# Kernel tuning notes

Measured on AMD Instinct MI355X. Metric: run time of the kernel, lower is better.

Reference implementation:

```python
import jax, jax.numpy as jnp
import numpy as np

ALPHA = 0.2          # LeakyReLU negative slope
NEG_INF = -9e15      # mask value used by the original module


def setup_inputs() -> dict:
    key = jax.random.key(0)
    k1, k2, k3, k4 = jax.random.split(key, 4)
    N, F_IN, F_OUT = 8192, 512, 256
    inp = jax.random.normal(k1, (N, F_IN), dtype=jnp.float32)
    W = jax.random.normal(k2, (F_IN, F_OUT), dtype=jnp.float32) * (1.414 / np.sqrt(F_IN))
    a = jax.random.normal(k3, (2 * F_OUT, 1), dtype=jnp.float32) * (1.414 / np.sqrt(F_OUT))
    adj = jax.random.randint(k4, (N, N), 0, 2, dtype=jnp.int32)
    return {"input": inp, "W": W, "a": a, "adj": adj}


def reference(input, W, a, adj):
    # h: [N, F_out]
    h = input @ W
    F_out = h.shape[1]
    # Original builds a_input[i,j] = concat(h_i, h_j) then matmuls with a.
    # Equivalent: e_ij = leakyrelu(h_i . a[:F] + h_j . a[F:]) without the O(N^2 * 2F) tensor.
    a1 = a[:F_out, 0]   # [F_out]
    a2 = a[F_out:, 0]   # [F_out]
    s1 = h @ a1         # [N]
    s2 = h @ a2         # [N]
    e = jax.nn.leaky_relu(s1[:, None] + s2[None, :], negative_slope=ALPHA)  # [N, N]
    attention = jax.nn.softmax(jnp.where(adj > 0, e, NEG_INF), axis=1)       # [N, N]
    return attention @ h  # [N, F_out]
```

## Files before the change

kernel.cpp:

```cpp
#include <hip/hip_runtime.h>


typedef __attribute__((ext_vector_type(8))) short bf16x8;
typedef __attribute__((ext_vector_type(4))) float fx4;
typedef __attribute__((ext_vector_type(4))) int ix4;
typedef __attribute__((ext_vector_type(2))) unsigned int ux2;

#define NN 8192
#define FIN 512
#define FOUT 256
#define PS 136
#define AROWS 32

__device__ __forceinline__ unsigned short f2bf(float f) {
    unsigned int x = __float_as_uint(f);
    x += 0x7fffu + ((x >> 16) & 1u);
    return (unsigned short)(x >> 16);
}
__device__ __forceinline__ bf16x8 pack8(fx4 a, fx4 b) {
    bf16x8 r;
    r[0] = (short)f2bf(a[0]); r[1] = (short)f2bf(a[1]);
    r[2] = (short)f2bf(a[2]); r[3] = (short)f2bf(a[3]);
    r[4] = (short)f2bf(b[0]); r[5] = (short)f2bf(b[1]);
    r[6] = (short)f2bf(b[2]); r[7] = (short)f2bf(b[3]);
    return r;
}

__global__ void wt_kernel(const float* __restrict__ W,
                          unsigned short* __restrict__ WTt) {
    const int c = threadIdx.x;
    const int k = blockIdx.x;
    WTt[((size_t)(k >> 5) * 256 + c) * 32 + (k & 31)] = f2bf(W[k * FOUT + c]);
}

__global__ __launch_bounds__(256) void prep_kernel(
    const float* __restrict__ X,
    const unsigned short* __restrict__ WTt,
    const float* __restrict__ A,
    unsigned short* __restrict__ hTt,
    float* __restrict__ s1, float* __restrict__ s2)
{
    __shared__ float s1sh[4][16], s2sh[4][16];
    const int tid = threadIdx.x;

    const int w = tid >> 6, l = tid & 63, q = l >> 4, lr = l & 15;
    const int r0 = blockIdx.x * 16;
    const int cbase = w * 64;
    fx4 acc[4] = {};

    for (int kb = 0; kb < FIN; kb += 32) {
        const float* xp = X + (size_t)(r0 + lr) * FIN + kb + q * 8;
        bf16x8 a0 = pack8(*(const fx4*)xp, *(const fx4*)(xp + 4));
#pragma unroll
        for (int tc = 0; tc < 4; ++tc) {
            bf16x8 b = *(const bf16x8*)(WTt + ((size_t)(kb >> 5) * 256 + cbase + tc * 16 + lr) * 32 + q * 8);
            acc[tc] = __builtin_amdgcn_mfma_f32_16x16x32_bf16(a0, b, acc[tc], 0, 0, 0);
        }
    }

    const int jb = r0 >> 5, jo = (r0 & 31) + q * 4;
#pragma unroll
    for (int tc = 0; tc < 4; ++tc) {
        const int c = cbase + tc * 16 + lr;
        ux2 hp;
        hp.x = (unsigned)f2bf(acc[tc][0]) | ((unsigned)f2bf(acc[tc][1]) << 16);
        hp.y = (unsigned)f2bf(acc[tc][2]) | ((unsigned)f2bf(acc[tc][3]) << 16);
        *(ux2*)(hTt + ((size_t)jb * 256 + c) * 32 + jo) = hp;
    }

    float p1[4] = {}, p2[4] = {};
#pragma unroll
    for (int tc = 0; tc < 4; ++tc) {
        const int c = cbase + tc * 16 + lr;
        const float a1v = A[c], a2v = A[FOUT + c];
#pragma unroll
        for (int r = 0; r < 4; ++r) {
            p1[r] += acc[tc][r] * a1v;
            p2[r] += acc[tc][r] * a2v;
        }
    }
#pragma unroll
    for (int r = 0; r < 4; ++r) {
#pragma unroll
        for (int off = 1; off < 16; off <<= 1) {
            p1[r] += __shfl_xor(p1[r], off);
            p2[r] += __shfl_xor(p2[r], off);
        }
        if (lr == 0) { s1sh[w][q * 4 + r] = p1[r]; s2sh[w][q * 4 + r] = p2[r]; }
    }
    __syncthreads();
    if (tid < 16) {
        s1[r0 + tid] = s1sh[0][tid] + s1sh[1][tid] + s1sh[2][tid] + s1sh[3][tid];
        s2[r0 + tid] = s2sh[0][tid] + s2sh[1][tid] + s2sh[2][tid] + s2sh[3][tid];
    }
}

__global__ __launch_bounds__(512) void attn_kernel(
    const int* __restrict__ adj,
    const unsigned short* __restrict__ hTt,
    const float* __restrict__ s1,
    const float* __restrict__ s2,
    float* __restrict__ out)
{
    __shared__ unsigned short P[2][AROWS * PS];
    __shared__ float dsh[AROWS];

    const int tid = threadIdx.x;
    const int r0 = blockIdx.x * AROWS;

    const int prow = tid >> 4;
    const int pq = tid & 15;
    const float s1v = s1[r0 + prow];
    const int* arow = adj + (size_t)(r0 + prow) * NN + pq * 8;
    float denp = 0.f;

    const int w = tid >> 6, l = tid & 63, q = l >> 4, lr = l & 15;
    const int cbase = w * 32;
    fx4 acc[2][2] = {};

    struct LSet { ix4 v0, v1; fx4 s2a, s2b; };
    LSet LA, LB;
    bf16x8 B0[4][2], B1[4][2];

    auto loadP = [&](int kt, LSet& L) {
        const int* ap = arow + kt * 128;
        L.v0 = __builtin_nontemporal_load((const ix4*)ap);
        L.v1 = __builtin_nontemporal_load((const ix4*)(ap + 4));
        L.s2a = *(const fx4*)(s2 + kt * 128 + pq * 8);
        L.s2b = *(const fx4*)(s2 + kt * 128 + pq * 8 + 4);
    };
    auto calcP = [&](int b, const LSet& L) {
        bf16x8 pv;
#pragma unroll
        for (int j = 0; j < 8; ++j) {
            const int aj = (j < 4) ? L.v0[j] : L.v1[j - 4];
            const float s2j = (j < 4) ? L.s2a[j] : L.s2b[j - 4];
            float t = s1v + s2j;
            float e = fmaxf(t, 0.2f * t);
            e = fminf(e, 30.f);
            const float p = (aj != 0) ? __expf(e) : 0.f;
            denp += p;
            pv[j] = (short)f2bf(p);
        }
        *(bf16x8*)(&P[b][prow * PS + pq * 8]) = pv;
    };
    auto loadB = [&](int it, bf16x8 (&B)[4][2]) {
#pragma unroll
        for (int ks = 0; ks < 4; ++ks)
#pragma unroll
            for (int tc = 0; tc < 2; ++tc)
                B[ks][tc] = *(const bf16x8*)(hTt + ((size_t)(it * 4 + ks) * 256 + cbase + tc * 16 + lr) * 32 + q * 8);
    };

    auto ldsBarrier = [&]() {
        asm volatile("s_waitcnt lgkmcnt(0)" ::: "memory");
        __builtin_amdgcn_s_barrier();
    };

    const int ITERS = NN / 128;
    loadP(0, LA);
    calcP(0, LA);
    loadP(1, LA);
    loadB(0, B0);
    ldsBarrier();

    auto body = [&](int it, bf16x8 (&Bc)[4][2], bf16x8 (&Bn)[4][2],
                    LSet& Lc, LSet& Ln) {
        if (it + 1 < ITERS) loadB(it + 1, Bn);
        if (it + 2 < ITERS) loadP(it + 2, Ln);
        const unsigned short* Pb = P[it & 1];
        bf16x8 af0[4], af1[4];
#pragma unroll
        for (int ks = 0; ks < 4; ++ks) {
            af0[ks] = *(const bf16x8*)(Pb + lr * PS + ks * 32 + q * 8);
            af1[ks] = *(const bf16x8*)(Pb + (16 + lr) * PS + ks * 32 + q * 8);
        }
        __builtin_amdgcn_s_setprio(1);
#pragma unroll
        for (int ks = 0; ks < 4; ++ks)
#pragma unroll
            for (int tc = 0; tc < 2; ++tc) {
                acc[0][tc] = __builtin_amdgcn_mfma_f32_16x16x32_bf16(af0[ks], Bc[ks][tc], acc[0][tc], 0, 0, 0);
                acc[1][tc] = __builtin_amdgcn_mfma_f32_16x16x32_bf16(af1[ks], Bc[ks][tc], acc[1][tc], 0, 0, 0);
            }
        __builtin_amdgcn_s_setprio(0);
        if (it + 1 < ITERS) calcP((it + 1) & 1, Lc);
        ldsBarrier();
    };

    for (int it = 0; it < ITERS; it += 2) {
        body(it, B0, B1, LA, LB);
        body(it + 1, B1, B0, LB, LA);
    }

    float v = denp;
    v += __shfl_xor(v, 1);
    v += __shfl_xor(v, 2);
    v += __shfl_xor(v, 4);
    v += __shfl_xor(v, 8);
    if (pq == 0) dsh[prow] = v;
    __syncthreads();

#pragma unroll
    for (int mg = 0; mg < 2; ++mg) {
#pragma unroll
        for (int r = 0; r < 4; ++r) {
            const int row = mg * 16 + q * 4 + r;
            const float dinv = 1.0f / fmaxf(dsh[row], 1e-30f);
#pragma unroll
            for (int tc = 0; tc < 2; ++tc) {
                out[(size_t)(r0 + row) * FOUT + cbase + tc * 16 + lr] = acc[mg][tc][r] * dinv;
            }
        }
    }
}

extern "C" void kernel_launch(void* const* d_in, const int* in_sizes, int n_in,
                              void* d_out, int out_size, void* d_ws, size_t ws_size,
                              hipStream_t stream) {
    const float *X = nullptr, *W = nullptr, *A = nullptr;
    const int* adj = nullptr;
    for (int i = 0; i < n_in; ++i) {
        switch (in_sizes[i]) {
            case NN * FIN:   X = (const float*)d_in[i]; break;
            case FIN * FOUT: W = (const float*)d_in[i]; break;
            case 2 * FOUT:   A = (const float*)d_in[i]; break;
            case NN * NN:    adj = (const int*)d_in[i]; break;
        }
    }
    if (!X) X = (const float*)d_in[0];
    if (!W) W = (const float*)d_in[1];
    if (!A) A = (const float*)d_in[2];
    if (!adj) adj = (const int*)d_in[3];
    float* out = (float*)d_out;

    char* ws = (char*)d_ws;
    float* s1 = (float*)ws;
    float* s2 = (float*)(ws + 32768);
    unsigned short* WTt = (unsigned short*)(ws + 98304);
    unsigned short* hTt = (unsigned short*)(ws + 360448);

    wt_kernel<<<512, 256, 0, stream>>>(W, WTt);
    prep_kernel<<<512, 256, 0, stream>>>(X, WTt, A, hTt, s1, s2);
    attn_kernel<<<NN / AROWS, 512, 0, stream>>>(adj, hTt, s1, s2, out);
}
```

Baseline: 442.4 us.

## Shrink attention tile to 16 rows with 256 threads and single-buffered B

Halves the attention block to 16 rows and 256 threads, so each wave covers 64 output columns (4 MFMA tiles) for one 16-row A fragment instead of two row groups over 32 columns. The B fragments of hTt are no longer double-buffered in registers but loaded at the start of each iteration, and the P computation for the next tile is moved ahead of the MFMAs to overlap it with those loads. This doubles the grid to 512 blocks and cuts register pressure, raising occupancy. The cost is that hTt is re-read twice as many times in total and B load latency is exposed within each iteration.

```diff
diff --git a/kernel.cpp b/kernel.cpp
--- a/kernel.cpp
+++ b/kernel.cpp
@@ -10,7 +10,7 @@
 #define FIN 512
 #define FOUT 256
 #define PS 136
-#define AROWS 32
+#define AROWS 16
 
 __device__ __forceinline__ unsigned short f2bf(float f) {
     unsigned int x = __float_as_uint(f);
@@ -95,7 +95,7 @@
     }
 }
 
-__global__ __launch_bounds__(512) void attn_kernel(
+__global__ __launch_bounds__(256) void attn_kernel(
     const int* __restrict__ adj,
     const unsigned short* __restrict__ hTt,
     const float* __restrict__ s1,
@@ -115,12 +115,12 @@
     float denp = 0.f;
 
     const int w = tid >> 6, l = tid & 63, q = l >> 4, lr = l & 15;
-    const int cbase = w * 32;
-    fx4 acc[2][2] = {};
+    const int cbase = w * 64;
+    fx4 acc[4] = {};
 
     struct LSet { ix4 v0, v1; fx4 s2a, s2b; };
     LSet LA, LB;
-    bf16x8 B0[4][2], B1[4][2];
+    bf16x8 B[4][4];
 
     auto loadP = [&](int kt, LSet& L) {
         const int* ap = arow + kt * 128;
@@ -144,11 +144,11 @@
         }
         *(bf16x8*)(&P[b][prow * PS + pq * 8]) = pv;
     };
-    auto loadB = [&](int it, bf16x8 (&B)[4][2]) {
+    auto loadB = [&](int it) {
 #pragma unroll
         for (int ks = 0; ks < 4; ++ks)
 #pragma unroll
-            for (int tc = 0; tc < 2; ++tc)
+            for (int tc = 0; tc < 4; ++tc)
                 B[ks][tc] = *(const bf16x8*)(hTt + ((size_t)(it * 4 + ks) * 256 + cbase + tc * 16 + lr) * 32 + q * 8);
     };
 
@@ -161,36 +161,30 @@
     loadP(0, LA);
     calcP(0, LA);
     loadP(1, LA);
-    loadB(0, B0);
     ldsBarrier();
 
-    auto body = [&](int it, bf16x8 (&Bc)[4][2], bf16x8 (&Bn)[4][2],
-                    LSet& Lc, LSet& Ln) {
-        if (it + 1 < ITERS) loadB(it + 1, Bn);
+    auto body = [&](int it, LSet& Lc, LSet& Ln) {
+        loadB(it);
         if (it + 2 < ITERS) loadP(it + 2, Ln);
         const unsigned short* Pb = P[it & 1];
-        bf16x8 af0[4], af1[4];
-#pragma unroll
-        for (int ks = 0; ks < 4; ++ks) {
+        bf16x8 af0[4];
+#pragma unroll
+        for (int ks = 0; ks < 4; ++ks)
             af0[ks] = *(const bf16x8*)(Pb + lr * PS + ks * 32 + q * 8);
-            af1[ks] = *(const bf16x8*)(Pb + (16 + lr) * PS + ks * 32 + q * 8);
-        }
+        if (it + 1 < ITERS) calcP((it + 1) & 1, Lc);
         __builtin_amdgcn_s_setprio(1);
 #pragma unroll
         for (int ks = 0; ks < 4; ++ks)
 #pragma unroll
-            for (int tc = 0; tc < 2; ++tc) {
-                acc[0][tc] = __builtin_amdgcn_mfma_f32_16x16x32_bf16(af0[ks], Bc[ks][tc], acc[0][tc], 0, 0, 0);
-                acc[1][tc] = __builtin_amdgcn_mfma_f32_16x16x32_bf16(af1[ks], Bc[ks][tc], acc[1][tc], 0, 0, 0);
-            }
+            for (int tc = 0; tc < 4; ++tc)
+                acc[tc] = __builtin_amdgcn_mfma_f32_16x16x32_bf16(af0[ks], B[ks][tc], acc[tc], 0, 0, 0);
         __builtin_amdgcn_s_setprio(0);
-        if (it + 1 < ITERS) calcP((it + 1) & 1, Lc);
         ldsBarrier();
     };
 
     for (int it = 0; it < ITERS; it += 2) {
-        body(it, B0, B1, LA, LB);
-        body(it + 1, B1, B0, LB, LA);
+        body(it, LA, LB);
+        body(it + 1, LB, LA);
     }
 
     float v = denp;
@@ -202,15 +196,12 @@
     __syncthreads();
 
 #pragma unroll
-    for (int mg = 0; mg < 2; ++mg) {
-#pragma unroll
-        for (int r = 0; r < 4; ++r) {
-            const int row = mg * 16 + q * 4 + r;
-            const float dinv = 1.0f / fmaxf(dsh[row], 1e-30f);
-#pragma unroll
-            for (int tc = 0; tc < 2; ++tc) {
-                out[(size_t)(r0 + row) * FOUT + cbase + tc * 16 + lr] = acc[mg][tc][r] * dinv;
-            }
+    for (int r = 0; r < 4; ++r) {
+        const int row = q * 4 + r;
+        const float dinv = 1.0f / fmaxf(dsh[row], 1e-30f);
+#pragma unroll
+        for (int tc = 0; tc < 4; ++tc) {
+            out[(size_t)(r0 + row) * FOUT + cbase + tc * 16 + lr] = acc[tc][r] * dinv;
         }
     }
 }
@@ -242,5 +233,5 @@
 
     wt_kernel<<<512, 256, 0, stream>>>(W, WTt);
     prep_kernel<<<512, 256, 0, stream>>>(X, WTt, A, hTt, s1, s2);
-    attn_kernel<<<NN / AROWS, 512, 0, stream>>>(adj, hTt, s1, s2, out);
-}
+    attn_kernel<<<NN / AROWS, 256, 0, stream>>>(adj, hTt, s1, s2, out);
+}
```

Result: slower. 478.2 us (+8.1%).

## Prefetch adjacency block into LDS bitmask before attention main loop

Applied to the files above, without the earlier changes.

Before the main loop, each block streams its 32 adjacency rows with wide nontemporal loads and packs them into a 32-bit-per-word bitmask held in LDS (about 33 KB). The softmax-numerator step then reads mask bits from LDS instead of issuing global int loads inside the pipelined loop. This separates the bandwidth-heavy adjacency read from the MFMA loop, but it serialises that read ahead of compute and raises LDS use per block, which may cut occupancy.

```diff
diff --git a/kernel.cpp b/kernel.cpp
--- a/kernel.cpp
+++ b/kernel.cpp
@@ -11,6 +11,7 @@
 #define FOUT 256
 #define PS 136
 #define AROWS 32
+#define MPAD 260
 
 __device__ __forceinline__ unsigned short f2bf(float f) {
     unsigned int x = __float_as_uint(f);
@@ -103,42 +104,60 @@
     float* __restrict__ out)
 {
     __shared__ unsigned short P[2][AROWS * PS];
+    __shared__ unsigned int mlds[AROWS * MPAD];
     __shared__ float dsh[AROWS];
 
     const int tid = threadIdx.x;
     const int r0 = blockIdx.x * AROWS;
+
+#pragma unroll 2
+    for (int s = 0; s < 16; ++s) {
+        const int g = s * 512 + tid;
+        const int row = g >> 8, dw = g & 255;
+        const int* base = adj + (size_t)(r0 + row) * NN + dw * 32;
+        ix4 v[8];
+#pragma unroll
+        for (int k = 0; k < 8; ++k)
+            v[k] = __builtin_nontemporal_load((const ix4*)(base + k * 4));
+        unsigned int m = 0;
+#pragma unroll
+        for (int k = 0; k < 8; ++k)
+#pragma unroll
+            for (int j = 0; j < 4; ++j)
+                m |= (v[k][j] != 0 ? 1u : 0u) << (k * 4 + j);
+        mlds[row * MPAD + dw] = m;
+    }
+    __syncthreads();
 
     const int prow = tid >> 4;
     const int pq = tid & 15;
     const float s1v = s1[r0 + prow];
-    const int* arow = adj + (size_t)(r0 + prow) * NN + pq * 8;
+    const int mshift = (pq & 3) * 8;
     float denp = 0.f;
 
     const int w = tid >> 6, l = tid & 63, q = l >> 4, lr = l & 15;
     const int cbase = w * 32;
     fx4 acc[2][2] = {};
 
-    struct LSet { ix4 v0, v1; fx4 s2a, s2b; };
+    struct LSet { fx4 s2a, s2b; };
     LSet LA, LB;
     bf16x8 B0[4][2], B1[4][2];
 
-    auto loadP = [&](int kt, LSet& L) {
-        const int* ap = arow + kt * 128;
-        L.v0 = __builtin_nontemporal_load((const ix4*)ap);
-        L.v1 = __builtin_nontemporal_load((const ix4*)(ap + 4));
+    auto loadS = [&](int kt, LSet& L) {
         L.s2a = *(const fx4*)(s2 + kt * 128 + pq * 8);
         L.s2b = *(const fx4*)(s2 + kt * 128 + pq * 8 + 4);
     };
-    auto calcP = [&](int b, const LSet& L) {
+    auto calcP = [&](int b, int kt, const LSet& L) {
+        const unsigned int mval = mlds[prow * MPAD + kt * 4 + (pq >> 2)];
+        const unsigned int mbyte = (mval >> mshift) & 0xFFu;
         bf16x8 pv;
 #pragma unroll
         for (int j = 0; j < 8; ++j) {
-            const int aj = (j < 4) ? L.v0[j] : L.v1[j - 4];
             const float s2j = (j < 4) ? L.s2a[j] : L.s2b[j - 4];
             float t = s1v + s2j;
             float e = fmaxf(t, 0.2f * t);
             e = fminf(e, 30.f);
-            const float p = (aj != 0) ? __expf(e) : 0.f;
+            const float p = ((mbyte >> j) & 1u) ? __expf(e) : 0.f;
             denp += p;
             pv[j] = (short)f2bf(p);
         }
@@ -158,16 +177,16 @@
     };
 
     const int ITERS = NN / 128;
-    loadP(0, LA);
-    calcP(0, LA);
-    loadP(1, LA);
+    loadS(0, LA);
+    calcP(0, 0, LA);
+    loadS(1, LA);
     loadB(0, B0);
     ldsBarrier();
 
     auto body = [&](int it, bf16x8 (&Bc)[4][2], bf16x8 (&Bn)[4][2],
                     LSet& Lc, LSet& Ln) {
         if (it + 1 < ITERS) loadB(it + 1, Bn);
-        if (it + 2 < ITERS) loadP(it + 2, Ln);
+        if (it + 2 < ITERS) loadS(it + 2, Ln);
         const unsigned short* Pb = P[it & 1];
         bf16x8 af0[4], af1[4];
 #pragma unroll
@@ -184,7 +203,7 @@
                 acc[1][tc] = __builtin_amdgcn_mfma_f32_16x16x32_bf16(af1[ks], Bc[ks][tc], acc[1][tc], 0, 0, 0);
             }
         __builtin_amdgcn_s_setprio(0);
-        if (it + 1 < ITERS) calcP((it + 1) & 1, Lc);
+        if (it + 1 < ITERS) calcP((it + 1) & 1, it + 1, Lc);
         ldsBarrier();
     };
 
```

Result: slower. 517.7 us (+17.0%).

## Split attention K-loop across two block halves with LDS reduction

Applied to the files above, without the earlier changes.

Doubles the attention block to 1024 threads. Each half processes half of the key dimension with its own double-buffered P tiles. Partial accumulators and softmax denominators are summed through shared memory in the epilogue. The goal is more waves in flight per CU to hide adjacency load latency, at the cost of extra LDS traffic, a larger block with register pressure under the 1024 launch bound, and a reduction step.

```diff
diff --git a/kernel.cpp b/kernel.cpp
--- a/kernel.cpp
+++ b/kernel.cpp
@@ -11,6 +11,7 @@
 #define FOUT 256
 #define PS 136
 #define AROWS 32
+#define ESTR 260
 
 __device__ __forceinline__ unsigned short f2bf(float f) {
     unsigned int x = __float_as_uint(f);
@@ -95,34 +96,37 @@
     }
 }
 
-__global__ __launch_bounds__(512) void attn_kernel(
+__global__ __launch_bounds__(1024) void attn_kernel(
     const int* __restrict__ adj,
     const unsigned short* __restrict__ hTt,
     const float* __restrict__ s1,
     const float* __restrict__ s2,
     float* __restrict__ out)
 {
-    __shared__ unsigned short P[2][AROWS * PS];
-    __shared__ float dsh[AROWS];
+    __shared__ unsigned short P[2][2][AROWS * PS];
+    __shared__ float dsh[2][AROWS];
 
     const int tid = threadIdx.x;
     const int r0 = blockIdx.x * AROWS;
-
-    const int prow = tid >> 4;
+    const int kh = tid >> 9;
+    const int khB = kh << 5;
+
+    const int prow = (tid >> 4) & 31;
     const int pq = tid & 15;
     const float s1v = s1[r0 + prow];
     const int* arow = adj + (size_t)(r0 + prow) * NN + pq * 8;
     float denp = 0.f;
 
     const int w = tid >> 6, l = tid & 63, q = l >> 4, lr = l & 15;
-    const int cbase = w * 32;
+    const int cbase = (w & 7) * 32;
     fx4 acc[2][2] = {};
 
     struct LSet { ix4 v0, v1; fx4 s2a, s2b; };
     LSet LA, LB;
     bf16x8 B0[4][2], B1[4][2];
 
-    auto loadP = [&](int kt, LSet& L) {
+    auto loadS = [&](int s, LSet& L) {
+        const int kt = khB + s;
         const int* ap = arow + kt * 128;
         L.v0 = __builtin_nontemporal_load((const ix4*)ap);
         L.v1 = __builtin_nontemporal_load((const ix4*)(ap + 4));
@@ -142,14 +146,15 @@
             denp += p;
             pv[j] = (short)f2bf(p);
         }
-        *(bf16x8*)(&P[b][prow * PS + pq * 8]) = pv;
-    };
-    auto loadB = [&](int it, bf16x8 (&B)[4][2]) {
+        *(bf16x8*)(&P[kh][b][prow * PS + pq * 8]) = pv;
+    };
+    auto loadB = [&](int s, bf16x8 (&B)[4][2]) {
+        const int kt = khB + s;
 #pragma unroll
         for (int ks = 0; ks < 4; ++ks)
 #pragma unroll
             for (int tc = 0; tc < 2; ++tc)
-                B[ks][tc] = *(const bf16x8*)(hTt + ((size_t)(it * 4 + ks) * 256 + cbase + tc * 16 + lr) * 32 + q * 8);
+                B[ks][tc] = *(const bf16x8*)(hTt + ((size_t)(kt * 4 + ks) * 256 + cbase + tc * 16 + lr) * 32 + q * 8);
     };
 
     auto ldsBarrier = [&]() {
@@ -157,18 +162,19 @@
         __builtin_amdgcn_s_barrier();
     };
 
-    const int ITERS = NN / 128;
-    loadP(0, LA);
+    const int STEPS = 32;
+
+    loadS(0, LA);
     calcP(0, LA);
-    loadP(1, LA);
+    loadS(1, LA);
     loadB(0, B0);
     ldsBarrier();
 
-    auto body = [&](int it, bf16x8 (&Bc)[4][2], bf16x8 (&Bn)[4][2],
+    auto body = [&](int s, bf16x8 (&Bc)[4][2], bf16x8 (&Bn)[4][2],
                     LSet& Lc, LSet& Ln) {
-        if (it + 1 < ITERS) loadB(it + 1, Bn);
-        if (it + 2 < ITERS) loadP(it + 2, Ln);
-        const unsigned short* Pb = P[it & 1];
+        if (s + 1 < STEPS) loadB(s + 1, Bn);
+        if (s + 2 < STEPS) loadS(s + 2, Ln);
+        const unsigned short* Pb = P[kh][s & 1];
         bf16x8 af0[4], af1[4];
 #pragma unroll
         for (int ks = 0; ks < 4; ++ks) {
@@ -184,13 +190,13 @@
                 acc[1][tc] = __builtin_amdgcn_mfma_f32_16x16x32_bf16(af1[ks], Bc[ks][tc], acc[1][tc], 0, 0, 0);
             }
         __builtin_amdgcn_s_setprio(0);
-        if (it + 1 < ITERS) calcP((it + 1) & 1, Lc);
+        if (s + 1 < STEPS) calcP((s + 1) & 1, Lc);
         ldsBarrier();
     };
 
-    for (int it = 0; it < ITERS; it += 2) {
-        body(it, B0, B1, LA, LB);
-        body(it + 1, B1, B0, LB, LA);
+    for (int s = 0; s < STEPS; s += 2) {
+        body(s, B0, B1, LA, LB);
+        body(s + 1, B1, B0, LB, LA);
     }
 
     float v = denp;
@@ -198,20 +204,37 @@
     v += __shfl_xor(v, 2);
     v += __shfl_xor(v, 4);
     v += __shfl_xor(v, 8);
-    if (pq == 0) dsh[prow] = v;
+    if (pq == 0) dsh[kh][prow] = v;
     __syncthreads();
 
-#pragma unroll
-    for (int mg = 0; mg < 2; ++mg) {
-#pragma unroll
-        for (int r = 0; r < 4; ++r) {
-            const int row = mg * 16 + q * 4 + r;
-            const float dinv = 1.0f / fmaxf(dsh[row], 1e-30f);
-#pragma unroll
-            for (int tc = 0; tc < 2; ++tc) {
-                out[(size_t)(r0 + row) * FOUT + cbase + tc * 16 + lr] = acc[mg][tc][r] * dinv;
+    float* epi = (float*)&P[0][0][0];
+    if (kh == 1) {
+#pragma unroll
+        for (int mg = 0; mg < 2; ++mg)
+#pragma unroll
+            for (int r = 0; r < 4; ++r) {
+                const int row = mg * 16 + q * 4 + r;
+#pragma unroll
+                for (int tc = 0; tc < 2; ++tc)
+                    epi[row * ESTR + cbase + tc * 16 + lr] = acc[mg][tc][r];
             }
-        }
+    }
+    __syncthreads();
+
+    if (kh == 0) {
+#pragma unroll
+        for (int mg = 0; mg < 2; ++mg)
+#pragma unroll
+            for (int r = 0; r < 4; ++r) {
+                const int row = mg * 16 + q * 4 + r;
+                const float dinv = 1.0f / fmaxf(dsh[0][row] + dsh[1][row], 1e-30f);
+#pragma unroll
+                for (int tc = 0; tc < 2; ++tc) {
+                    const int col = cbase + tc * 16 + lr;
+                    out[(size_t)(r0 + row) * FOUT + col] =
+                        (acc[mg][tc][r] + epi[row * ESTR + col]) * dinv;
+                }
+            }
     }
 }
 
@@ -242,5 +265,5 @@
 
     wt_kernel<<<512, 256, 0, stream>>>(W, WTt);
     prep_kernel<<<512, 256, 0, stream>>>(X, WTt, A, hTt, s1, s2);
-    attn_kernel<<<NN / AROWS, 512, 0, stream>>>(adj, hTt, s1, s2, out);
-}
+    attn_kernel<<<NN / AROWS, 1024, 0, stream>>>(adj, hTt, s1, s2, out);
+}
```

After: 701.1 us. +58.5%, slower.
